# Kernel optimization log

Measured on AMD Instinct MI355X. Metric: run time of the kernel, lower is better.

Reference implementation:

```python
import math
import jax, jax.numpy as jnp
import numpy as np

GROUPS = 32
EPS = 1e-5


def group_norm(x, gamma, beta):
    # x: (b, c, h, w); normalize per-group over (c/g, h, w)
    b, c, h, w = x.shape
    xg = x.reshape(b, GROUPS, c // GROUPS, h, w)
    mu = xg.mean(axis=(2, 3, 4), keepdims=True)
    var = xg.var(axis=(2, 3, 4), keepdims=True)
    xn = ((xg - mu) * jax.lax.rsqrt(var + EPS)).reshape(b, c, h, w)
    return xn * gamma[None, :, None, None] + beta[None, :, None, None]


def conv1x1(x, w, bias):
    # x: (b, c, h, w), w: (o, c) -> (b, o, h, w)
    return jnp.einsum('bchw,oc->bohw', x, w) + bias[None, :, None, None]


def setup_inputs() -> dict:
    key = jax.random.key(0)
    ks = jax.random.split(key, 7)
    b, c, h, w = 8, 512, 32, 32
    s = 1.0 / math.sqrt(c)
    return {
        'x': jax.random.normal(ks[0], (b, c, h, w), dtype=jnp.float32),
        'gn_w': jnp.ones((c,), dtype=jnp.float32),
        'gn_b': jnp.zeros((c,), dtype=jnp.float32),
        'qkv_w': jax.random.normal(ks[1], (3 * c, c), dtype=jnp.float32) * s,
        'qkv_b': jnp.zeros((3 * c,), dtype=jnp.float32),
        'proj_w': jax.random.normal(ks[2], (c, c), dtype=jnp.float32) * s,
        'proj_b': jnp.zeros((c,), dtype=jnp.float32),
        'num_heads': 8,
    }


def reference(x, gn_w, gn_b, qkv_w, qkv_b, proj_w, proj_b, num_heads):
    b, c, h, w = x.shape
    hds = num_heads
    d = c // hds
    x_ = group_norm(x, gn_w, gn_b)
    qkv = conv1x1(x_, qkv_w, qkv_b)  # (b, 3c, h, w)
    q, k, v = jnp.split(qkv, 3, axis=1)
    # (b, hds, d, hw)
    q = q.reshape(b, hds, d, h * w)
    k = k.reshape(b, hds, d, h * w)
    v = v.reshape(b, hds, d, h * w)
    # scores: (b, hds, hw, hw) = q^T k / sqrt(d)
    scores = jnp.einsum('bhdq,bhdk->bhqk', q, k) / math.sqrt(d)
    attn = jax.nn.softmax(scores, axis=-1)
    # out = (attn @ v^T)^T -> (b, hds, d, hw)
    out = jnp.einsum('bhqk,bhdk->bhdq', attn, v)
    out = out.reshape(b, c, h, w)
    return x + conv1x1(out, proj_w, proj_b)
```

## Files before the change

kernel.cpp:

```cpp
#include <hip/hip_runtime.h>
#include <hip/hip_bf16.h>


typedef __attribute__((ext_vector_type(8))) short short8v;
typedef __attribute__((ext_vector_type(4))) short short4v;
typedef __attribute__((ext_vector_type(4))) float f32x4;
typedef __attribute__((ext_vector_type(2))) unsigned uint2v;
typedef __attribute__((ext_vector_type(4))) unsigned uint4v;

constexpr int Bn = 8, Cn = 512, HWn = 1024;

#if __has_builtin(__builtin_amdgcn_exp2f)
#define EXP2F(x) __builtin_amdgcn_exp2f(x)
#else
#define EXP2F(x) __exp2f(x)
#endif

static __device__ __forceinline__ unsigned short bf16u(float f) {
  __hip_bfloat16 h = __float2bfloat16(f);
  return __builtin_bit_cast(unsigned short, h);
}
static __device__ __forceinline__ short bf16_of(float f) {
  return (short)bf16u(f);
}
static __device__ __forceinline__ unsigned bf16pk(float a, float b) {
  return (unsigned)bf16u(a) | ((unsigned)bf16u(b) << 16);
}
static __device__ __forceinline__ unsigned cvtpk(float lo, float hi) {
  unsigned r;
  asm("v_cvt_pk_bf16_f32 %0, %1, %2" : "=v"(r) : "v"(lo), "v"(hi));
  return r;
}

static __device__ __forceinline__ void gload16(const void* g, void* l) {
  __builtin_amdgcn_global_load_lds(
      (const __attribute__((address_space(1))) unsigned*)g,
      (__attribute__((address_space(3))) unsigned*)l, 16, 0, 0);
}

__global__ __launch_bounds__(256) void gn_fused_k(const float* __restrict__ x,
                                                  const float* __restrict__ gw,
                                                  const float* __restrict__ gb,
                                                  const float* __restrict__ wq,
                                                  const float* __restrict__ wp,
                                                  short* __restrict__ oq,
                                                  short* __restrict__ op,
                                                  short* __restrict__ xn3) {
  const int t = threadIdx.x;
  if (blockIdx.x >= 256) {
    int i = (blockIdx.x - 256) * 256 + t;
    const float* src = wq;
    short* dst = oq;
    int idx = i;
    if (i >= 196608) { src = wp; dst = op; idx = i - 196608; }
    f32x4 v = ((const f32x4*)src)[idx];
    short4v o;
    o.x = bf16_of(v.x); o.y = bf16_of(v.y); o.z = bf16_of(v.z); o.w = bf16_of(v.w);
    *(short4v*)&dst[idx * 4] = o;
    return;
  }
  const int bg = blockIdx.x;
  const int g = bg & 31;
  const f32x4* src = (const f32x4*)(x + (size_t)bg * 16384);
  f32x4 v[16];
  float s = 0.f, ss = 0.f;
#pragma unroll
  for (int k = 0; k < 16; k++) {
    v[k] = src[t + 256 * k];
    s += v[k].x + v[k].y + v[k].z + v[k].w;
    ss += v[k].x * v[k].x + v[k].y * v[k].y + v[k].z * v[k].z + v[k].w * v[k].w;
  }
#pragma unroll
  for (int off = 32; off; off >>= 1) {
    s += __shfl_xor(s, off);
    ss += __shfl_xor(ss, off);
  }
  __shared__ float rs[4], rss[4];
  const int lane = t & 63, w = t >> 6;
  if (lane == 0) { rs[w] = s; rss[w] = ss; }
  __syncthreads();
  const float S = rs[0] + rs[1] + rs[2] + rs[3];
  const float SS = rss[0] + rss[1] + rss[2] + rss[3];
  constexpr float invn = 1.0f / 16384.f;
  const float mu = S * invn;
  const float var = SS * invn - mu * mu;
  const float rstd = rsqrtf(var + 1e-5f);
  float ga[16], be[16];
#pragma unroll
  for (int k = 0; k < 16; k++) {
    ga[k] = gw[g * 16 + k] * rstd;
    be[k] = gb[g * 16 + k] - mu * ga[k];
  }
  short* dst = xn3 + (size_t)bg * 16384;
#pragma unroll
  for (int d = 0; d < 4; d++) {
    unsigned pk[8];
#pragma unroll
    for (int k = 0; k < 16; k += 2)
      pk[k >> 1] = bf16pk(fmaf(v[k][d], ga[k], be[k]),
                          fmaf(v[k + 1][d], ga[k + 1], be[k + 1]));
    uint4v lo = {pk[0], pk[1], pk[2], pk[3]};
    uint4v hi = {pk[4], pk[5], pk[6], pk[7]};
    *(uint4v*)&dst[(4 * t + d) * 16] = lo;
    *(uint4v*)&dst[(4 * t + d) * 16 + 8] = hi;
  }
}

__device__ __forceinline__ short8v frag64(const short* buf, int row, int gk) {
  return *(const short8v*)&buf[row * 64 + ((gk ^ (row & 7)) << 3)];
}
__device__ __forceinline__ short8v frag128(const short* buf, int row, int gk) {
  return *(const short8v*)&buf[row * 128 + ((gk ^ (row & 7)) << 3)];
}

__global__ __launch_bounds__(256, 2) void gemm_qkv_k(
    const short* __restrict__ A, const short* __restrict__ xn3,
    const float* __restrict__ bias, short* __restrict__ oQ,
    short* __restrict__ oK, short* __restrict__ oV) {
  const int bid = blockIdx.x;
  const int swz = (bid & 7) * 96 + (bid >> 3);
  const int bn = swz & 7;
  const int rest = swz >> 3;
  const int bm = rest % 12, b = rest / 12;
  const bool VBLK = (bm >= 8);

  const short* Bb = xn3 + (size_t)b * 524288;
  __shared__ __align__(16) short As[2][8192];
  __shared__ __align__(16) short Bs[2][8192];
  const int t = threadIdx.x, l = t & 63, w = t >> 6;
  const int wr = w >> 1, wc = w & 1;
  const int m0 = bm * 128, n0 = bn * 128;
  const f32x4 vzero = {0.f, 0.f, 0.f, 0.f};
  f32x4 acc[4][4];
#pragma unroll
  for (int i = 0; i < 4; i++)
#pragma unroll
    for (int j = 0; j < 4; j++) acc[i][j] = vzero;

  const int sr0 = t >> 3;
  const int sg = t & 7;

#define STAGE_QKV(buf, k0)                                                    \
  do {                                                                        \
    _Pragma("unroll") for (int it = 0; it < 4; it++) {                        \
      int r = it * 32 + sr0;                                                  \
      int gs = sg ^ (r & 7);                                                  \
      gload16(&A[(size_t)(m0 + r) * 512 + (k0) + gs * 8],                     \
              &As[buf][it * 2048 + w * 512]);                                 \
      int gp = ((k0) >> 4) + (gs >> 1);                                       \
      gload16(&Bb[(size_t)((gp << 10) + n0 + r) * 16 + ((gs & 1) << 3)],      \
              &Bs[buf][it * 2048 + w * 512]);                                 \
    }                                                                         \
  } while (0)

  STAGE_QKV(0, 0);
  __syncthreads();

  for (int ks = 0; ks < 8; ks++) {
    const int cb = ks & 1;
    if (ks < 7) STAGE_QKV(cb ^ 1, (ks + 1) * 64);
#pragma unroll
    for (int kk = 0; kk < 2; kk++) {
      short8v af[4], bf[4];
#pragma unroll
      for (int i = 0; i < 4; i++)
        af[i] = frag64(&As[cb][0], wr * 64 + i * 16 + (l & 15), kk * 4 + (l >> 4));
#pragma unroll
      for (int j = 0; j < 4; j++)
        bf[j] = frag64(&Bs[cb][0], wc * 64 + j * 16 + (l & 15), kk * 4 + (l >> 4));
      if (VBLK) {
#pragma unroll
        for (int i = 0; i < 4; i++)
#pragma unroll
          for (int j = 0; j < 4; j++)
            acc[i][j] = __builtin_amdgcn_mfma_f32_16x16x32_bf16(bf[j], af[i], acc[i][j], 0, 0, 0);
      } else {
#pragma unroll
        for (int i = 0; i < 4; i++)
#pragma unroll
          for (int j = 0; j < 4; j++)
            acc[i][j] = __builtin_amdgcn_mfma_f32_16x16x32_bf16(af[i], bf[j], acc[i][j], 0, 0, 0);
      }
    }
    __syncthreads();
  }

  if (!VBLK) {
    short* oBase = (m0 < 512) ? oQ : oK;
    const int mc = (m0 < 512 ? m0 : m0 - 512) + wr * 64;
#pragma unroll
    for (int i = 0; i < 4; i++) {
      int mi = mc + i * 16 + (l >> 4) * 4;
      f32x4 bv = *(const f32x4*)&bias[m0 + wr * 64 + i * 16 + (l >> 4) * 4];
#pragma unroll
      for (int j = 0; j < 4; j++) {
        int n = n0 + wc * 64 + j * 16 + (l & 15);
        uint2v pk = {bf16pk(acc[i][j][0] + bv[0], acc[i][j][1] + bv[1]),
                     bf16pk(acc[i][j][2] + bv[2], acc[i][j][3] + bv[3])};
        *(uint2v*)&oBase[((size_t)b * HWn + n) * 512 + mi] = pk;
      }
    }
  } else {
#pragma unroll
    for (int i = 0; i < 4; i++) {
      int m = m0 + wr * 64 + i * 16 + (l & 15);
      float bv = bias[m];
      short* vrow = oV + ((size_t)b * 512 + (m - 1024)) * HWn;
#pragma unroll
      for (int j = 0; j < 4; j++) {
        int n = n0 + wc * 64 + j * 16 + (l >> 4) * 4;
        uint2v pk = {bf16pk(acc[i][j][0] + bv, acc[i][j][1] + bv),
                     bf16pk(acc[i][j][2] + bv, acc[i][j][3] + bv)};
        *(uint2v*)&vrow[n] = pk;
      }
    }
  }
}

__global__ __launch_bounds__(512, 2) void gemm_proj_k(
    const short* __restrict__ A, const short* __restrict__ Bt,
    const float* __restrict__ bias, const float* __restrict__ resid,
    float* __restrict__ outF) {
  const int bid = blockIdx.x;
  const int swz = (bid & 7) * 32 + (bid >> 3);
  const int bn = swz & 7;
  const int rest = swz >> 3;
  const int bm = rest & 3, b = rest >> 2;

  const short* Bb = Bt + (size_t)b * HWn * Cn;
  __shared__ __align__(16) short As[2][8192];
  __shared__ __align__(16) short Bs[2][8192];
  const int t = threadIdx.x, l = t & 63, w = t >> 6;
  const int wr = w >> 1, wc = w & 1;
  const int m0 = bm * 128, n0 = bn * 128;
  const f32x4 vzero = {0.f, 0.f, 0.f, 0.f};
  f32x4 acc[2][4];
#pragma unroll
  for (int i = 0; i < 2; i++)
#pragma unroll
    for (int j = 0; j < 4; j++) acc[i][j] = vzero;

  const int sr0 = t >> 3;
  const int sg = t & 7;

#define STAGE_PROJ(buf, k0)                                                   \
  do {                                                                        \
    _Pragma("unroll") for (int it = 0; it < 2; it++) {                        \
      int r = it * 64 + sr0;                                                  \
      int gs = sg ^ (r & 7);                                                  \
      gload16(&A[(size_t)(m0 + r) * 512 + (k0) + gs * 8],                     \
              &As[buf][it * 4096 + w * 512]);                                 \
      gload16(&Bb[(size_t)(n0 + r) * 512 + (k0) + gs * 8],                    \
              &Bs[buf][it * 4096 + w * 512]);                                 \
    }                                                                         \
  } while (0)

  STAGE_PROJ(0, 0);
  __syncthreads();

  for (int ks = 0; ks < 8; ks++) {
    const int cb = ks & 1;
    if (ks < 7) STAGE_PROJ(cb ^ 1, (ks + 1) * 64);
#pragma unroll
    for (int kk = 0; kk < 2; kk++) {
      short8v af[2], bf[4];
#pragma unroll
      for (int i = 0; i < 2; i++)
        af[i] = frag64(&As[cb][0], wr * 32 + i * 16 + (l & 15), kk * 4 + (l >> 4));
#pragma unroll
      for (int j = 0; j < 4; j++)
        bf[j] = frag64(&Bs[cb][0], wc * 64 + j * 16 + (l & 15), kk * 4 + (l >> 4));
#pragma unroll
      for (int i = 0; i < 2; i++)
#pragma unroll
        for (int j = 0; j < 4; j++)
          acc[i][j] = __builtin_amdgcn_mfma_f32_16x16x32_bf16(af[i], bf[j], acc[i][j], 0, 0, 0);
    }
    __syncthreads();
  }

  float* outb = outF + (size_t)b * Cn * HWn;
  const float* rb = resid + (size_t)b * Cn * HWn;
#pragma unroll
  for (int i = 0; i < 2; i++) {
    f32x4 bv = *(const f32x4*)&bias[m0 + wr * 32 + i * 16 + (l >> 4) * 4];
#pragma unroll
    for (int r = 0; r < 4; r++) {
      int m = m0 + wr * 32 + i * 16 + (l >> 4) * 4 + r;
#pragma unroll
      for (int j = 0; j < 4; j++) {
        int n = n0 + wc * 64 + j * 16 + (l & 15);
        size_t idx = (size_t)m * HWn + n;
        outb[idx] = acc[i][j][r] + bv[r] + rb[idx];
      }
    }
  }
}

__global__ __launch_bounds__(256, 2) void attn_k(const short* __restrict__ qT,
                                                 const short* __restrict__ kT,
                                                 const short* __restrict__ vB,
                                                 short* __restrict__ aoT) {
  const int bid = blockIdx.x;
  const int swz = (bid & 7) * 64 + (bid >> 3);
  const int qt = swz & 7, head = (swz >> 3) & 7, b = swz >> 6;
  __shared__ __align__(16) short SM[33792];
  short* Ks = SM;
  short* Vs = SM + 8192;
  short* Ps = SM + 16384;
  const int t = threadIdx.x, l = t & 63, w = t >> 6;
  short* PsA = Ps + (2 * w) * 2176;
  short* PsB = Ps + (2 * w + 1) * 2176;
  const int g = l >> 4;
  const f32x4 vzero = {0.f, 0.f, 0.f, 0.f};

  const short* ksrc = kT + (size_t)b * HWn * 512 + head * 64;
  const short* vsrc = vB + ((size_t)b * 512 + head * 64) * HWn;

  const short* qbase = qT +
      ((size_t)b * HWn + qt * 128 + 32 * w + (l & 15)) * 512 + head * 64 + g * 8;
  const short8v qA0 = *(const short8v*)&qbase[0];
  const short8v qA1 = *(const short8v*)&qbase[32];
  const short8v qB0 = *(const short8v*)&qbase[16 * 512];
  const short8v qB1 = *(const short8v*)&qbase[16 * 512 + 32];

  const int kkv0 = w * 8 + (l >> 3), kg = l & 7;
  const int vd0 = w * 4 + (l >> 4), vg = l & 15;

#pragma unroll
  for (int it = 0; it < 4; it++) {
    int kv = kkv0 + it * 32;
    gload16(&ksrc[(size_t)kv * 512 + (kg ^ (kv & 7)) * 8], &Ks[it * 2048 + w * 512]);
    int d = vd0 + it * 16;
    gload16(&vsrc[(size_t)d * HWn + (vg ^ (d & 7)) * 8], &Vs[it * 2048 + w * 512]);
  }
  __syncthreads();

  f32x4 oaA[4], oaB[4];
#pragma unroll
  for (int f = 0; f < 4; f++) { oaA[f] = vzero; oaB[f] = vzero; }
  float lA = 0.f, lB = 0.f;
  constexpr float SC = 0.1803368801111f;
  constexpr float MOFF = -11.5415602855f;

#pragma unroll 1
  for (int kt = 0; kt < 8; kt++) {
    short8v kreg[4], vreg[4];
    if (kt < 7) {
      const int kt1 = kt + 1;
#pragma unroll
      for (int it = 0; it < 4; it++) {
        int kv = kkv0 + it * 32;
        kreg[it] = *(const short8v*)&ksrc[(size_t)(kt1 * 128 + kv) * 512 +
                                          (kg ^ (kv & 7)) * 8];
        int d = vd0 + it * 16;
        vreg[it] = *(const short8v*)&vsrc[(size_t)d * HWn + kt1 * 128 +
                                          (vg ^ (d & 7)) * 8];
      }
    }

    f32x4 saA[8], saB[8];
    __builtin_amdgcn_s_setprio(1);
#pragma unroll
    for (int f = 0; f < 8; f++) {
      short8v ka0 = frag64(Ks, 16 * f + (l & 15), g);
      short8v ka1 = frag64(Ks, 16 * f + (l & 15), g + 4);
      saA[f] = __builtin_amdgcn_mfma_f32_16x16x32_bf16(ka0, qA0, vzero, 0, 0, 0);
      saB[f] = __builtin_amdgcn_mfma_f32_16x16x32_bf16(ka0, qB0, vzero, 0, 0, 0);
      saA[f] = __builtin_amdgcn_mfma_f32_16x16x32_bf16(ka1, qA1, saA[f], 0, 0, 0);
      saB[f] = __builtin_amdgcn_mfma_f32_16x16x32_bf16(ka1, qB1, saB[f], 0, 0, 0);
    }
    __builtin_amdgcn_s_setprio(0);

    f32x4 psAv = vzero, psBv = vzero;
#pragma unroll
    for (int f = 0; f < 8; f++)
#pragma unroll
      for (int r = 0; r < 4; r++) {
        float eA = EXP2F(fmaf(saA[f][r], SC, MOFF));
        float eB = EXP2F(fmaf(saB[f][r], SC, MOFF));
        saA[f][r] = eA;
        saB[f][r] = eB;
        psAv[r] += eA;
        psBv[r] += eB;
      }
    float psA = (psAv[0] + psAv[1]) + (psAv[2] + psAv[3]);
    float psB = (psBv[0] + psBv[1]) + (psBv[2] + psBv[3]);
    psA += __shfl_xor(psA, 16);
    psA += __shfl_xor(psA, 32);
    psB += __shfl_xor(psB, 16);
    psB += __shfl_xor(psB, 32);
    lA += psA;
    lB += psB;

    short8v paA[4], paB[4];
#pragma unroll
    for (int c = 0; c < 4; c++) {
      unsigned A0 = cvtpk(saA[2 * c][0], saA[2 * c][1]);
      unsigned A1 = cvtpk(saA[2 * c][2], saA[2 * c][3]);
      unsigned B0 = cvtpk(saA[2 * c + 1][0], saA[2 * c + 1][1]);
      unsigned B1 = cvtpk(saA[2 * c + 1][2], saA[2 * c + 1][3]);
      uint2v p0 = __builtin_amdgcn_permlane32_swap(A0, B0, false, false);
      uint2v p1 = __builtin_amdgcn_permlane32_swap(A1, B1, false, false);
      uint2v q0 = __builtin_amdgcn_permlane16_swap(p0[0], p0[1], false, false);
      uint2v q1 = __builtin_amdgcn_permlane16_swap(p1[0], p1[1], false, false);
      uint4v ua = {q0[0], q1[0], q0[1], q1[1]};
      paA[c] = __builtin_bit_cast(short8v, ua);

      unsigned C0 = cvtpk(saB[2 * c][0], saB[2 * c][1]);
      unsigned C1 = cvtpk(saB[2 * c][2], saB[2 * c][3]);
      unsigned D0 = cvtpk(saB[2 * c + 1][0], saB[2 * c + 1][1]);
      unsigned D1 = cvtpk(saB[2 * c + 1][2], saB[2 * c + 1][3]);
      uint2v p2 = __builtin_amdgcn_permlane32_swap(C0, D0, false, false);
      uint2v p3 = __builtin_amdgcn_permlane32_swap(C1, D1, false, false);
      uint2v q2 = __builtin_amdgcn_permlane16_swap(p2[0], p2[1], false, false);
      uint2v q3 = __builtin_amdgcn_permlane16_swap(p3[0], p3[1], false, false);
      uint4v ub = {q2[0], q3[0], q2[1], q3[1]};
      paB[c] = __builtin_bit_cast(short8v, ub);
    }

    __builtin_amdgcn_s_setprio(1);
#pragma unroll
    for (int fd = 0; fd < 4; fd++) {
      int row = 16 * fd + (l & 15);
#pragma unroll
      for (int c = 0; c < 4; c++) {
        short8v vb = frag128(Vs, row, c * 4 + g);
        oaA[fd] = __builtin_amdgcn_mfma_f32_16x16x32_bf16(paA[c], vb, oaA[fd], 0, 0, 0);
        oaB[fd] = __builtin_amdgcn_mfma_f32_16x16x32_bf16(paB[c], vb, oaB[fd], 0, 0, 0);
      }
    }
    __builtin_amdgcn_s_setprio(0);

    if (kt < 7) {
      __syncthreads();
#pragma unroll
      for (int it = 0; it < 4; it++) {
        *(short8v*)&Ks[it * 2048 + w * 512 + l * 8] = kreg[it];
        *(short8v*)&Vs[it * 2048 + w * 512 + l * 8] = vreg[it];
      }
      __syncthreads();
    }
  }

  const float invA = 1.0f / lA, invB = 1.0f / lB;
  float ivA[4], ivB[4];
#pragma unroll
  for (int r = 0; r < 4; r++) {
    ivA[r] = __shfl(invA, 4 * g + r);
    ivB[r] = __shfl(invB, 4 * g + r);
  }
#pragma unroll
  for (int r = 0; r < 4; r++)
#pragma unroll
    for (int f = 0; f < 4; f++) {
      PsA[(4 * g + r) * 136 + 16 * f + (l & 15)] = bf16_of(oaA[f][r] * ivA[r]);
      PsB[(4 * g + r) * 136 + 16 * f + (l & 15)] = bf16_of(oaB[f][r] * ivB[r]);
    }
  __syncthreads();
  short* dst = aoT + ((size_t)b * HWn + qt * 128) * 512 + head * 64;
#pragma unroll
  for (int it = 0; it < 4; it++) {
    int r = (t >> 3) + 32 * it;
    int c8 = (t & 7) * 8;
    *(short8v*)&dst[(size_t)r * 512 + c8] =
        *(const short8v*)&Ps[(r >> 4) * 2176 + (r & 15) * 136 + c8];
  }
}

extern "C" void kernel_launch(void* const* d_in, const int* in_sizes, int n_in,
                              void* d_out, int out_size, void* d_ws, size_t ws_size,
                              hipStream_t stream) {
  const float* x = (const float*)d_in[0];
  const float* gn_w = (const float*)d_in[1];
  const float* gn_b = (const float*)d_in[2];
  const float* qkv_w = (const float*)d_in[3];
  const float* qkv_b = (const float*)d_in[4];
  const float* proj_w = (const float*)d_in[5];
  const float* proj_b = (const float*)d_in[6];
  float* out = (float*)d_out;

  char* ws = (char*)d_ws;
  short* wqb = (short*)(ws + 4096);
  short* wpb = (short*)(ws + 4096 + 1572864);
  char* p = ws + 4096 + 1572864 + 524288;
  const size_t SB = (size_t)Bn * HWn * 512 * 2;
  short* xn3 = (short*)p;
  short* qT = (short*)(p + SB);
  short* kT = (short*)(p + 2 * SB);
  short* vB = (short*)(p + 3 * SB);
  short* aoT = (short*)(p + 4 * SB);

  gn_fused_k<<<1280, 256, 0, stream>>>(x, gn_w, gn_b, qkv_w, proj_w, wqb, wpb, xn3);
  gemm_qkv_k<<<768, 256, 0, stream>>>(wqb, xn3, qkv_b, qT, kT, vB);
  attn_k<<<512, 256, 0, stream>>>(qT, kT, vB, aoT);
  gemm_proj_k<<<256, 512, 0, stream>>>(wpb, aoT, proj_b, x, out);
}
```

Baseline: 75.30 us.

## Double-buffer K/V tiles in LDS with direct global-to-LDS loads

The attention kernel used to prefetch the next K/V tile into registers and copy it into a single LDS buffer between two barriers. It now splits LDS into two K/V buffers and issues direct global-to-LDS loads for tile kt+1 into the idle buffer while tile kt is computed, leaving one barrier per iteration. The output staging area now reuses the same LDS behind an extra barrier, which also shrinks the shared allocation. This is meant to cut register pressure and barrier stalls and to overlap loads with MFMA work. In exchange it relies on the async loads finishing before the per-iteration barrier.

```diff
diff --git a/kernel.cpp b/kernel.cpp
--- a/kernel.cpp
+++ b/kernel.cpp
@@ -304,13 +304,8 @@
   const int bid = blockIdx.x;
   const int swz = (bid & 7) * 64 + (bid >> 3);
   const int qt = swz & 7, head = (swz >> 3) & 7, b = swz >> 6;
-  __shared__ __align__(16) short SM[33792];
-  short* Ks = SM;
-  short* Vs = SM + 8192;
-  short* Ps = SM + 16384;
+  __shared__ __align__(16) short SM[32768];
   const int t = threadIdx.x, l = t & 63, w = t >> 6;
-  short* PsA = Ps + (2 * w) * 2176;
-  short* PsB = Ps + (2 * w + 1) * 2176;
   const int g = l >> 4;
   const f32x4 vzero = {0.f, 0.f, 0.f, 0.f};
 
@@ -327,13 +322,19 @@
   const int kkv0 = w * 8 + (l >> 3), kg = l & 7;
   const int vd0 = w * 4 + (l >> 4), vg = l & 15;
 
-#pragma unroll
-  for (int it = 0; it < 4; it++) {
-    int kv = kkv0 + it * 32;
-    gload16(&ksrc[(size_t)kv * 512 + (kg ^ (kv & 7)) * 8], &Ks[it * 2048 + w * 512]);
-    int d = vd0 + it * 16;
-    gload16(&vsrc[(size_t)d * HWn + (vg ^ (d & 7)) * 8], &Vs[it * 2048 + w * 512]);
-  }
+#define STAGE_KV(bp, kt_)                                                     \
+  do {                                                                        \
+    _Pragma("unroll") for (int it = 0; it < 4; it++) {                        \
+      int kv = kkv0 + it * 32;                                                \
+      gload16(&ksrc[(size_t)((kt_) * 128 + kv) * 512 + (kg ^ (kv & 7)) * 8],  \
+              &SM[(bp) + it * 2048 + w * 512]);                               \
+      int d = vd0 + it * 16;                                                  \
+      gload16(&vsrc[(size_t)d * HWn + (kt_) * 128 + (vg ^ (d & 7)) * 8],      \
+              &SM[(bp) + 8192 + it * 2048 + w * 512]);                        \
+    }                                                                         \
+  } while (0)
+
+  STAGE_KV(0, 0);
   __syncthreads();
 
   f32x4 oaA[4], oaB[4];
@@ -345,19 +346,10 @@
 
 #pragma unroll 1
   for (int kt = 0; kt < 8; kt++) {
-    short8v kreg[4], vreg[4];
-    if (kt < 7) {
-      const int kt1 = kt + 1;
-#pragma unroll
-      for (int it = 0; it < 4; it++) {
-        int kv = kkv0 + it * 32;
-        kreg[it] = *(const short8v*)&ksrc[(size_t)(kt1 * 128 + kv) * 512 +
-                                          (kg ^ (kv & 7)) * 8];
-        int d = vd0 + it * 16;
-        vreg[it] = *(const short8v*)&vsrc[(size_t)d * HWn + kt1 * 128 +
-                                          (vg ^ (d & 7)) * 8];
-      }
-    }
+    const int cb = (kt & 1) * 16384;
+    if (kt < 7) STAGE_KV(cb ^ 16384, kt + 1);
+    const short* Ks = SM + cb;
+    const short* Vs = SM + cb + 8192;
 
     f32x4 saA[8], saB[8];
     __builtin_amdgcn_s_setprio(1);
@@ -432,15 +424,7 @@
     }
     __builtin_amdgcn_s_setprio(0);
 
-    if (kt < 7) {
-      __syncthreads();
-#pragma unroll
-      for (int it = 0; it < 4; it++) {
-        *(short8v*)&Ks[it * 2048 + w * 512 + l * 8] = kreg[it];
-        *(short8v*)&Vs[it * 2048 + w * 512 + l * 8] = vreg[it];
-      }
-      __syncthreads();
-    }
+    if (kt < 7) __syncthreads();
   }
 
   const float invA = 1.0f / lA, invB = 1.0f / lB;
@@ -450,6 +434,9 @@
     ivA[r] = __shfl(invA, 4 * g + r);
     ivB[r] = __shfl(invB, 4 * g + r);
   }
+  __syncthreads();
+  short* PsA = SM + (2 * w) * 2176;
+  short* PsB = SM + (2 * w + 1) * 2176;
 #pragma unroll
   for (int r = 0; r < 4; r++)
 #pragma unroll
@@ -464,7 +451,7 @@
     int r = (t >> 3) + 32 * it;
     int c8 = (t & 7) * 8;
     *(short8v*)&dst[(size_t)r * 512 + c8] =
-        *(const short8v*)&Ps[(r >> 4) * 2176 + (r & 15) * 136 + c8];
+        *(const short8v*)&SM[(r >> 4) * 2176 + (r & 15) * 136 + c8];
   }
 }
 
```

Result: no change. 75.31 us (+0.0%).
